# Optimization experiments

Measured on AMD Instinct MI355X. Metric: run time of the kernel, lower is better.

Reference implementation:

```python
import jax, jax.numpy as jnp
import numpy as np

N = 4096   # nodes
G = 64     # graphs
MH = 128   # hidden multiplicity (0e and 1o)
MU = 64    # up multiplicity (0e and 1o)
NSP = 10   # num_species
EPS = 1e-5


def _forward(nfh, nfu, onehot, W_h0, W_h1, W_u0, W_u1, Wt_00, Wt_11, Wt_01, Wt_10,
             W_p0, b_p0, W_p1, Wsc0, Wsc1, ln_w0, ln_b0, ln_w1, W_s0, b_s0, W_s1, batch):
    n = nfh.shape[0]
    # unpack irreps layout: [0e scalars | 1o vectors flattened]
    h0 = nfh[:, :MH]                       # [N, MH]
    h1 = nfh[:, MH:].reshape(n, MH, 3)     # [N, MH, 3]
    u0 = nfu[:, :MU]
    u1 = nfu[:, MU:].reshape(n, MU, 3)
    inv_h = 1.0 / np.sqrt(MH)
    inv_u = 1.0 / np.sqrt(MU)
    # irrep-wise (block-diagonal) o3.Linear, e3nn fan-in normalization
    hp0 = (h0 @ W_h0) * inv_h
    hp1 = jnp.einsum('nui,uv->nvi', h1, W_h1) * inv_h
    up0 = (u0 @ W_u0) * inv_u
    up1 = jnp.einsum('nui,uv->nvi', u1, W_u1) * inv_u
    # SeparateWeightTensorProduct: fully-connected 'uvw' CG tensor product
    # paths to 0e (scalars + gates, 2*MH outputs): 0e x 0e and 1o x 1o (dot / sqrt3)
    inv_tp = 1.0 / np.sqrt(2.0 * MH * MU)   # component/path normalization (2 paths, fan MH*MU)
    xy00 = jnp.einsum('nu,nv->nuv', hp0, up0).reshape(n, MH * MU)
    xy11 = jnp.einsum('nui,nvi->nuv', hp1, up1).reshape(n, MH * MU)
    z0 = (xy00 @ Wt_00.reshape(MH * MU, 2 * MH)
          + (xy11 @ Wt_11.reshape(MH * MU, 2 * MH)) / np.sqrt(3.0)) * inv_tp  # [N, 2*MH]
    # paths to 1o: 0e x 1o and 1o x 0e (staged to control intermediate size)
    ta = jnp.einsum('nu,uvw->nvw', hp0, Wt_01)       # [N, MU, MH]
    z1a = jnp.einsum('nvw,nvi->nwi', ta, up1)
    tb = jnp.einsum('nv,uvw->nuw', up0, Wt_10)       # [N, MH, MH]
    z1b = jnp.einsum('nuw,nui->nwi', tb, hp1)
    z1 = (z1a + z1b) * inv_tp                        # [N, MH, 3]
    # Gate nonlinearity: silu on scalars, sigmoid gates multiply 1o features
    s = jax.nn.silu(z0[:, :MH])
    g = jax.nn.sigmoid(z0[:, MH:])
    v = z1 * g[:, :, None]
    # lin_post (biases on scalars only)
    p0 = (s @ W_p0) * inv_h + b_p0
    p1 = jnp.einsum('nui,uv->nvi', v, W_p1) * inv_h
    # self-connection: FullyConnectedTensorProduct(hidden, NSPx0e, out)
    inv_sc = 1.0 / np.sqrt(MH * NSP)
    sxy0 = jnp.einsum('nu,nv->nuv', h0, onehot).reshape(n, MH * NSP)
    y0 = p0 + (sxy0 @ Wsc0.reshape(MH * NSP, MH)) * inv_sc
    sxy1 = jnp.einsum('nui,nv->nuvi', h1, onehot).reshape(n, MH * NSP, 3)
    y1 = p1 + jnp.einsum('nki,kw->nwi', sxy1, Wsc1.reshape(MH * NSP, MH)) * inv_sc
    # e3LayerNorm: per-graph stats; mean-subtract scalars only, RMS-normalize per irrep
    ones = jnp.ones((n,), y0.dtype)
    cnt = jnp.maximum(jax.ops.segment_sum(ones, batch, num_segments=G), 1.0)[:, None]
    mean0 = (jax.ops.segment_sum(y0, batch, num_segments=G) / cnt).mean(axis=1)  # [G]
    f0 = y0 - mean0[batch][:, None]
    var0 = (jax.ops.segment_sum(f0 * f0, batch, num_segments=G) / cnt).mean(axis=1)
    f0 = f0 / (jnp.sqrt(var0)[batch][:, None] + EPS) * ln_w0 + ln_b0
    var1 = (jax.ops.segment_sum((y1 * y1).reshape(n, -1), batch, num_segments=G) / cnt).mean(axis=1)
    f1 = y1 / (jnp.sqrt(var1)[batch][:, None, None] + EPS) * ln_w1[None, :, None]
    # residual skip connection (o3.Linear with scalar bias)
    out0 = f0 + (h0 @ W_s0) * inv_h + b_s0
    out1 = f1 + jnp.einsum('nui,uv->nvi', h1, W_s1) * inv_h
    return jnp.concatenate([out0, out1.reshape(n, 3 * MH)], axis=1)  # [N, 512]


def setup_inputs() -> dict:
    key = jax.random.key(0)
    ks = jax.random.split(key, 20)
    f = lambda i, shape: jax.random.normal(ks[i], shape, dtype=jnp.float32)
    species = jax.random.randint(ks[0], (N,), 0, NSP)
    return {
        'node_feats_hidden': f(1, (N, 4 * MH)),
        'node_feats_up': f(2, (N, 4 * MU)),
        'node_one_hot': jax.nn.one_hot(species, NSP, dtype=jnp.float32),
        'batch': jnp.sort(jax.random.randint(ks[3], (N,), 0, G)),
        'W_h0': f(4, (MH, MH)), 'W_h1': f(5, (MH, MH)),
        'W_u0': f(6, (MU, MU)), 'W_u1': f(7, (MU, MU)),
        'Wt_00': f(8, (MH, MU, 2 * MH)), 'Wt_11': f(9, (MH, MU, 2 * MH)),
        'Wt_01': f(10, (MH, MU, MH)), 'Wt_10': f(11, (MH, MU, MH)),
        'W_p0': f(12, (MH, MH)), 'b_p0': jnp.zeros((MH,), jnp.float32), 'W_p1': f(13, (MH, MH)),
        'Wsc0': f(14, (MH, NSP, MH)), 'Wsc1': f(15, (MH, NSP, MH)),
        'ln_w0': jnp.ones((MH,), jnp.float32), 'ln_b0': jnp.zeros((MH,), jnp.float32),
        'ln_w1': jnp.ones((MH,), jnp.float32),
        'W_s0': f(16, (MH, MH)), 'b_s0': jnp.zeros((MH,), jnp.float32), 'W_s1': f(17, (MH, MH)),
    }


def reference(node_feats_hidden, node_feats_up, node_one_hot, batch, W_h0, W_h1, W_u0, W_u1,
              Wt_00, Wt_11, Wt_01, Wt_10, W_p0, b_p0, W_p1, Wsc0, Wsc1, ln_w0, ln_b0, ln_w1,
              W_s0, b_s0, W_s1):
    return _forward(node_feats_hidden, node_feats_up, node_one_hot, W_h0, W_h1, W_u0, W_u1,
                    Wt_00, Wt_11, Wt_01, Wt_10, W_p0, b_p0, W_p1, Wsc0, Wsc1,
                    ln_w0, ln_b0, ln_w1, W_s0, b_s0, W_s1, batch)
```

## Files before the change

### kernel.cpp

```cpp
#include <hip/hip_runtime.h>
#include <cstdint>
#include <cstddef>


typedef _Float16 half8 __attribute__((ext_vector_type(8)));
typedef _Float16 half4v __attribute__((ext_vector_type(4)));
typedef float f32x4 __attribute__((ext_vector_type(4)));

static constexpr float INV_H  = 0.08838834764831845f;
static constexpr float INV_U  = 0.125f;
static constexpr float INV_TP = 0.0078125f;
static constexpr float INV_SC = 0.02795084971874737f;
static constexpr float RSQRT3 = 0.5773502691896258f;
static constexpr float LN_EPS = 1e-5f;

static constexpr size_t OFF_BZ0 = 0;
static constexpr size_t OFF_BZ1 = OFF_BZ0 + 8388608;
static constexpr size_t OFF_WH0 = OFF_BZ1 + 4194304;
static constexpr size_t OFF_WH1 = OFF_WH0 + 32768;
static constexpr size_t OFF_WU0 = OFF_WH1 + 32768;
static constexpr size_t OFF_WU1 = OFF_WU0 + 8192;
static constexpr size_t OFF_WP0 = OFF_WU1 + 8192;
static constexpr size_t OFF_WP1 = OFF_WP0 + 32768;
static constexpr size_t OFF_WS0 = OFF_WP1 + 32768;
static constexpr size_t OFF_WS1 = OFF_WS0 + 32768;
static constexpr size_t OFF_H0F = OFF_WS1 + 32768;
static constexpr size_t OFF_H1F = OFF_H0F + 1048576;
static constexpr size_t OFF_U0F = OFF_H1F + 3145728;
static constexpr size_t OFF_U1F = OFF_U0F + 524288;
static constexpr size_t OFF_HP0 = OFF_U1F + 1572864;
static constexpr size_t OFF_HP1 = OFF_HP0 + 1048576;
static constexpr size_t OFF_UP0 = OFF_HP1 + 3145728;
static constexpr size_t OFF_UP1 = OFF_UP0 + 524288;
static constexpr size_t OFF_SF  = OFF_UP1 + 1572864;
static constexpr size_t OFF_VF  = OFF_SF + 1048576;
static constexpr size_t OFF_PZ0 = OFF_VF + 3145728;
static constexpr size_t OFF_PZ1 = OFF_PZ0 + 16777216;
static constexpr size_t OFF_Y0  = OFF_PZ1 + 12582912;
static constexpr size_t OFF_Y1  = OFF_Y0 + 2097152;
static constexpr size_t OFF_O0  = OFF_Y1 + 6291456;
static constexpr size_t OFF_O1  = OFF_O0 + 2097152;
static constexpr size_t OFF_SP  = OFF_O1 + 6291456;
static constexpr size_t OFF_ST  = OFF_SP + 16384;
static constexpr size_t WS_NEED = OFF_ST + 2048;

__global__ __launch_bounds__(256) void kconv(
    const float* __restrict__ nfh, const float* __restrict__ nfu,
    const float* __restrict__ onehot,
    const float* __restrict__ Wt00, const float* __restrict__ Wt11,
    const float* __restrict__ Wt01, const float* __restrict__ Wt10,
    const float* __restrict__ Wh0, const float* __restrict__ Wh1,
    const float* __restrict__ Wu0, const float* __restrict__ Wu1,
    const float* __restrict__ Wp0, const float* __restrict__ Wp1,
    const float* __restrict__ Ws0, const float* __restrict__ Ws1,
    char* __restrict__ ws)
{
  const int bid = blockIdx.x, t = threadIdx.x;
  if (bid < 768) {
    __shared__ float lds[64 * 130];
    _Float16* dst;
    int u, nt = 0;
    const bool isz0 = bid < 512;
    if (isz0) { nt = bid >> 8; u = bid & 255; dst = (_Float16*)(ws + OFF_BZ0) + ((size_t)nt*256 + (size_t)u)*8192; }
    else      { u = bid - 512;               dst = (_Float16*)(ws + OFF_BZ1) + (size_t)u*8192; }

    const float* src; int rowpitch, c0; float scale = 1.f;
    if (isz0) {
      rowpitch = 256; c0 = nt*128;
      if (u < 128) { src = Wt00 + (size_t)(u*64)*256; }
      else         { src = Wt11 + (size_t)((u-128)*64)*256; scale = RSQRT3; }
    } else {
      rowpitch = 128; c0 = 0;
      if (u < 128) { src = Wt01 + (size_t)(u*64)*128; }
      else         { src = Wt10 + (size_t)((u-128)*64)*128; }
    }

    #pragma unroll
    for (int it = 0; it < 8; ++it) {
      int gi = it*256 + t;
      int row = gi >> 5, c4 = gi & 31;
      const float4 v = *(const float4*)(src + (size_t)row*rowpitch + c0 + c4*4);
      float* dl = lds + row*130 + c4*4;
      dl[0] = v.x; dl[1] = v.y; dl[2] = v.z; dl[3] = v.w;
    }
    __syncthreads();

    for (int it = 0; it < 4; ++it) {
      int chunk = it*256 + t;
      int lane = chunk & 63, ch = chunk >> 6;
      int f = ch >> 1, c = ch & 1;
      int w = f*16 + (lane & 15);
      int v0 = c*32 + (lane >> 4)*8;
      half8 o;
      #pragma unroll
      for (int j = 0; j < 8; ++j)
        o[j] = (_Float16)(lds[(v0 + j)*130 + w] * scale);
      *(half8*)(dst + (size_t)chunk*8) = o;
    }
  } else if (bid < 776) {
    int mat = bid - 768;
    const float* src; size_t doff; int K, N;
    switch (mat) {
      case 0: src = Wh0; doff = OFF_WH0; K = 128; N = 128; break;
      case 1: src = Wh1; doff = OFF_WH1; K = 128; N = 128; break;
      case 2: src = Wu0; doff = OFF_WU0; K = 64;  N = 64;  break;
      case 3: src = Wu1; doff = OFF_WU1; K = 64;  N = 64;  break;
      case 4: src = Wp0; doff = OFF_WP0; K = 128; N = 128; break;
      case 5: src = Wp1; doff = OFF_WP1; K = 128; N = 128; break;
      case 6: src = Ws0; doff = OFF_WS0; K = 128; N = 128; break;
      default: src = Ws1; doff = OFF_WS1; K = 128; N = 128; break;
    }
    _Float16* d = (_Float16*)(ws + doff);
    const int nfr = N >> 4;
    const int chunks = (K*N) >> 3;
    for (int qd = t; qd < chunks; qd += 256) {
      int lane = qd & 63, cf = qd >> 6;
      int f = cf % nfr, c = cf / nfr;
      int col = f*16 + (lane & 15);
      int k0 = c*32 + (lane >> 4)*8;
      half8 o;
      #pragma unroll
      for (int j = 0; j < 8; ++j) o[j] = (_Float16)src[(size_t)(k0 + j)*N + col];
      *(half8*)(d + (size_t)qd*8) = o;
    }
  } else if (bid < 1544) {
    const int stride = 768*256;
    const int base = (bid - 776)*256 + t;
    _Float16* h0f = (_Float16*)(ws + OFF_H0F);
    _Float16* h1f = (_Float16*)(ws + OFF_H1F);
    _Float16* u0f = (_Float16*)(ws + OFF_U0F);
    _Float16* u1f = (_Float16*)(ws + OFF_U1F);
    for (int vid = base; vid < 131072; vid += stride) {
      int n = vid >> 5, c4 = (vid & 31)*4;
      const float4 v = *(const float4*)(nfh + (size_t)n*512 + c4);
      half4v o = { (_Float16)v.x, (_Float16)v.y, (_Float16)v.z, (_Float16)v.w };
      *(half4v*)(h0f + (size_t)vid*4) = o;
    }
    for (int vid = base; vid < 65536; vid += stride) {
      int n = vid >> 4, c4 = (vid & 15)*4;
      const float4 v = *(const float4*)(nfu + (size_t)n*256 + c4);
      half4v o = { (_Float16)v.x, (_Float16)v.y, (_Float16)v.z, (_Float16)v.w };
      *(half4v*)(u0f + (size_t)vid*4) = o;
    }
    for (int id = base; id < 524288; id += stride) {
      int n = id >> 7, u = id & 127;
      const float* s = nfh + (size_t)n*512 + 128 + u*3;
      h1f[id]            = (_Float16)s[0];
      h1f[524288 + id]   = (_Float16)s[1];
      h1f[1048576 + id]  = (_Float16)s[2];
    }
    for (int id = base; id < 262144; id += stride) {
      int n = id >> 6, v = id & 63;
      const float* s = nfu + (size_t)n*256 + 64 + v*3;
      u1f[id]            = (_Float16)s[0];
      u1f[262144 + id]   = (_Float16)s[1];
      u1f[524288 + id]   = (_Float16)s[2];
    }
  } else {
    int node = (bid - 1544)*256 + t;
    const float* row = onehot + (size_t)node*10;
    int best = 0; float bv = row[0];
    #pragma unroll
    for (int s = 1; s < 10; ++s) { float v = row[s]; if (v > bv) { bv = v; best = s; } }
    ((int*)(ws + OFF_SP))[node] = best;
    if (bid == 1544) {
      float* stz = (float*)(ws + OFF_ST);
      stz[t] = 0.f; stz[t + 256] = 0.f;
    }
  }
}

template<int KK, int NO, int MODE>
__device__ __forceinline__ void gemm_small_body(char* __restrict__ ws,
    const float* __restrict__ bp0, const float* __restrict__ bs0,
    int bid, int t)
{
  constexpr int NT = NO / 16;
  const int lane = t & 63, wid = t >> 6;
  const int quad = lane >> 4, l15 = lane & 15;
  const int job = bid >> 5, n0 = (bid & 31) << 7;

  const _Float16 *A, *W;
  _Float16* oh = nullptr; float* of = nullptr;
  const float* bias = nullptr;
  float scale;
  if constexpr (MODE == 0) {
    scale = INV_H;
    if (job == 0) { A = (const _Float16*)(ws + OFF_H0F); W = (const _Float16*)(ws + OFF_WH0); oh = (_Float16*)(ws + OFF_HP0); }
    else {
      A = (const _Float16*)(ws + OFF_H1F) + (size_t)(job-1)*524288;
      W = (const _Float16*)(ws + OFF_WH1);
      oh = (_Float16*)(ws + OFF_HP1) + (size_t)(job-1)*524288;
    }
  } else if constexpr (MODE == 1) {
    scale = INV_U;
    if (job == 0) { A = (const _Float16*)(ws + OFF_U0F); W = (const _Float16*)(ws + OFF_WU0); oh = (_Float16*)(ws + OFF_UP0); }
    else {
      A = (const _Float16*)(ws + OFF_U1F) + (size_t)(job-1)*262144;
      W = (const _Float16*)(ws + OFF_WU1);
      oh = (_Float16*)(ws + OFF_UP1) + (size_t)(job-1)*262144;
    }
  } else {
    scale = INV_H;
    switch (job) {
      case 0: A = (const _Float16*)(ws + OFF_SF);  W = (const _Float16*)(ws + OFF_WP0); of = (float*)(ws + OFF_Y0); bias = bp0; break;
      case 1: A = (const _Float16*)(ws + OFF_H0F); W = (const _Float16*)(ws + OFF_WS0); of = (float*)(ws + OFF_O0); bias = bs0; break;
      case 2: case 3: case 4:
        A = (const _Float16*)(ws + OFF_VF) + (size_t)(job-2)*524288;
        W = (const _Float16*)(ws + OFF_WP1);
        of = (float*)(ws + OFF_Y1) + (size_t)(job-2)*524288; break;
      default:
        A = (const _Float16*)(ws + OFF_H1F) + (size_t)(job-5)*524288;
        W = (const _Float16*)(ws + OFF_WS1);
        of = (float*)(ws + OFF_O1) + (size_t)(job-5)*524288; break;
    }
  }

  f32x4 acc[2][NT];
  const f32x4 zz = {0.f, 0.f, 0.f, 0.f};
  #pragma unroll
  for (int mf = 0; mf < 2; ++mf)
    #pragma unroll
    for (int nf = 0; nf < NT; ++nf) acc[mf][nf] = zz;

  #pragma unroll
  for (int kc = 0; kc < KK/32; ++kc) {
    half8 a[2];
    #pragma unroll
    for (int mf = 0; mf < 2; ++mf)
      a[mf] = *(const half8*)(A + (size_t)(n0 + wid*32 + mf*16 + l15)*KK + kc*32 + quad*8);
    #pragma unroll
    for (int nf = 0; nf < NT; ++nf) {
      half8 b = *(const half8*)(W + (size_t)(kc*NT + nf)*512 + lane*8);
      #pragma unroll
      for (int mf = 0; mf < 2; ++mf)
        acc[mf][nf] = __builtin_amdgcn_mfma_f32_16x16x32_f16(a[mf], b, acc[mf][nf], 0, 0, 0);
    }
  }

  #pragma unroll
  for (int mf = 0; mf < 2; ++mf)
    #pragma unroll
    for (int nf = 0; nf < NT; ++nf) {
      int col = nf*16 + l15;
      float bv = bias ? bias[col] : 0.f;
      #pragma unroll
      for (int r = 0; r < 4; ++r) {
        int row = n0 + wid*32 + mf*16 + quad*4 + r;
        float v = acc[mf][nf][r] * scale + bv;
        if constexpr (MODE < 2) oh[(size_t)row*NO + col] = (_Float16)v;
        else                    of[(size_t)row*NO + col] = v;
      }
    }
}

__global__ __launch_bounds__(256) void kprep(char* __restrict__ ws)
{
  if (blockIdx.x < 128) gemm_small_body<128,128,0>(ws, nullptr, nullptr, blockIdx.x, threadIdx.x);
  else                  gemm_small_body<64, 64, 1>(ws, nullptr, nullptr, blockIdx.x - 128, threadIdx.x);
}

__global__ __launch_bounds__(256) void ktail(char* __restrict__ ws,
    const float* __restrict__ bp0, const float* __restrict__ bs0)
{
  gemm_small_body<128,128,2>(ws, bp0, bs0, blockIdx.x, threadIdx.x);
}

__global__ __launch_bounds__(256, 2) void kbig(char* __restrict__ ws)
{
  const int bid = blockIdx.x, t = threadIdx.x;
  const int lane = t & 63, wid = t >> 6;
  const int wy = wid >> 1, wx = wid & 1;
  const int quad = lane >> 4, l15 = lane & 15;

  const _Float16* hp0 = (const _Float16*)(ws + OFF_HP0);
  const _Float16* hp1 = (const _Float16*)(ws + OFF_HP1);
  const _Float16* up0 = (const _Float16*)(ws + OFF_UP0);
  const _Float16* up1 = (const _Float16*)(ws + OFF_UP1);

  const _Float16 *p, *q, *B0;
  _Float16* out; int opitch; size_t obase; int node0;
  if (bid < 256) {
    int mt = bid >> 3, nt = (bid >> 2) & 1, kj = bid & 3;
    node0 = mt << 7;
    if (kj == 0) { p = hp0; q = up0; }
    else { p = hp1 + (size_t)(kj-1)*524288; q = up1 + (size_t)(kj-1)*262144; }
    B0 = (const _Float16*)(ws + OFF_BZ0) + (size_t)nt*2097152 + (kj ? (size_t)1048576 : (size_t)0);
    out = (_Float16*)(ws + OFF_PZ0) + (size_t)kj*1048576;
    obase = (size_t)node0*256 + (size_t)nt*128;
    opitch = 256;
  } else {
    int b2 = bid - 256, mt = b2 >> 1, kj = b2 & 1, i = mt >> 5;
    node0 = (mt & 31) << 7;
    if (kj == 0) { p = hp0; q = up1 + (size_t)i*262144; }
    else         { p = hp1 + (size_t)i*524288; q = up0; }
    B0 = (const _Float16*)(ws + OFF_BZ1) + (kj ? (size_t)1048576 : (size_t)0);
    out = (_Float16*)(ws + OFF_PZ1) + (size_t)kj*1572864;
    obase = (size_t)mt*16384;
    opitch = 128;
  }

  half8 qf[4][2];
  #pragma unroll
  for (int mf = 0; mf < 4; ++mf)
    #pragma unroll
    for (int c = 0; c < 2; ++c)
      qf[mf][c] = *(const half8*)(q + (size_t)(node0 + wy*64 + mf*16 + l15)*64 + c*32 + quad*8);

  f32x4 acc[4][4];
  const f32x4 zz = {0.f, 0.f, 0.f, 0.f};
  #pragma unroll
  for (int mf = 0; mf < 4; ++mf)
    #pragma unroll
    for (int nf = 0; nf < 4; ++nf) acc[mf][nf] = zz;

  const _Float16* prow = p + (size_t)(node0 + wy*64 + l15)*128;
  const _Float16* Bw = B0 + (size_t)wx*4096 + (size_t)lane*8;

  for (int u4 = 0; u4 < 32; ++u4) {
    half4v pw[4];
    #pragma unroll
    for (int mf = 0; mf < 4; ++mf)
      pw[mf] = *(const half4v*)(prow + (size_t)mf*2048 + u4*4);
    #pragma unroll
    for (int uu = 0; uu < 4; ++uu) {
      const _Float16* Bu = Bw + (size_t)(u4*4 + uu)*8192;
      half8 bf[2][4];
      #pragma unroll
      for (int c = 0; c < 2; ++c)
        #pragma unroll
        for (int nf = 0; nf < 4; ++nf)
          bf[c][nf] = *(const half8*)(Bu + (size_t)((nf*2 + c)*512));
      #pragma unroll
      for (int mf = 0; mf < 4; ++mf) {
        const _Float16 ps = pw[mf][uu];
        const half8 pv = {ps, ps, ps, ps, ps, ps, ps, ps};
        #pragma unroll
        for (int c = 0; c < 2; ++c) {
          half8 a = qf[mf][c] * pv;
          #pragma unroll
          for (int nf = 0; nf < 4; ++nf)
            acc[mf][nf] = __builtin_amdgcn_mfma_f32_16x16x32_f16(a, bf[c][nf], acc[mf][nf], 0, 0, 0);
        }
      }
    }
  }

  #pragma unroll
  for (int mf = 0; mf < 4; ++mf)
    #pragma unroll
    for (int nf = 0; nf < 4; ++nf) {
      int col = wx*64 + nf*16 + l15;
      #pragma unroll
      for (int r = 0; r < 4; ++r) {
        int row = wy*64 + mf*16 + quad*4 + r;
        out[obase + (size_t)row*opitch + col] = (_Float16)acc[mf][nf][r];
      }
    }
}

__global__ __launch_bounds__(256) void kreduce(char* __restrict__ ws)
{
  const int id = blockIdx.x*256 + threadIdx.x;
  const int n = id >> 7, w = id & 127;
  const _Float16* pz0 = (const _Float16*)(ws + OFF_PZ0);
  const _Float16* pz1 = (const _Float16*)(ws + OFF_PZ1);
  _Float16* sf = (_Float16*)(ws + OFF_SF);
  _Float16* vf = (_Float16*)(ws + OFF_VF);
  const size_t b = (size_t)n*256;
  float zs = ((float)pz0[b + w] + (float)pz0[1048576 + b + w]
            + (float)pz0[2097152 + b + w] + (float)pz0[3145728 + b + w]) * INV_TP;
  float zg = ((float)pz0[b + 128 + w] + (float)pz0[1048576 + b + 128 + w]
            + (float)pz0[2097152 + b + 128 + w] + (float)pz0[3145728 + b + 128 + w]) * INV_TP;
  float s = zs / (1.f + __expf(-zs));
  float g = 1.f / (1.f + __expf(-zg));
  sf[id] = (_Float16)s;
  #pragma unroll
  for (int i = 0; i < 3; ++i) {
    size_t r = ((size_t)i*4096 + (size_t)n)*128 + w;
    float z1v = ((float)pz1[r] + (float)pz1[1572864 + r]) * INV_TP;
    vf[(size_t)i*524288 + (size_t)n*128 + w] = (_Float16)(z1v * g);
  }
}

__global__ __launch_bounds__(256) void kscstats(char* __restrict__ ws,
    const float* __restrict__ nfh,
    const float* __restrict__ Wsc0, const float* __restrict__ Wsc1,
    const int* __restrict__ batch)
{
  const int t = threadIdx.x;
  const int node = blockIdx.x*2 + (t >> 7);
  const int w = t & 127;
  const int sp = ((const int*)(ws + OFF_SP))[node];
  const float* h = nfh + (size_t)node*512;
  float a0 = 0.f, a10 = 0.f, a11 = 0.f, a12 = 0.f;
  for (int u = 0; u < 128; ++u) {
    const size_t wi = (size_t)(u*10 + sp)*128 + w;
    float w0 = Wsc0[wi];
    float w1 = Wsc1[wi];
    a0 += h[u] * w0;
    a10 += h[128 + u*3 + 0] * w1;
    a11 += h[128 + u*3 + 1] * w1;
    a12 += h[128 + u*3 + 2] * w1;
  }
  float* y0 = (float*)(ws + OFF_Y0);
  float* y1 = (float*)(ws + OFF_Y1);
  const size_t i0 = (size_t)node*128 + w;
  float y0n  = y0[i0]           + INV_SC * a0;
  float y1n0 = y1[i0]           + INV_SC * a10;
  float y1n1 = y1[524288 + i0]  + INV_SC * a11;
  float y1n2 = y1[1048576 + i0] + INV_SC * a12;
  y0[i0] = y0n;
  y1[i0] = y1n0;
  y1[524288 + i0]  = y1n1;
  y1[1048576 + i0] = y1n2;

  float s0 = y0n, ss0 = y0n*y0n, ss1 = y1n0*y1n0 + y1n1*y1n1 + y1n2*y1n2;
  #pragma unroll
  for (int m = 1; m < 64; m <<= 1) {
    s0  += __shfl_xor(s0, m, 64);
    ss0 += __shfl_xor(ss0, m, 64);
    ss1 += __shfl_xor(ss1, m, 64);
  }
  __shared__ float red[4][3];
  if ((t & 63) == 0) {
    red[t >> 6][0] = s0; red[t >> 6][1] = ss0; red[t >> 6][2] = ss1;
  }
  __syncthreads();
  if ((t & 127) == 0) {
    const int wv = t >> 6;
    float* stp = (float*)(ws + OFF_ST);
    const int g = batch[node];
    atomicAdd(&stp[g],       red[wv][0] + red[wv+1][0]);
    atomicAdd(&stp[64 + g],  red[wv][1] + red[wv+1][1]);
    atomicAdd(&stp[128 + g], red[wv][2] + red[wv+1][2]);
    atomicAdd(&stp[192 + g], 1.f);
  }
}

__global__ __launch_bounds__(256) void kfinal(char* __restrict__ ws, const int* __restrict__ batch,
    const float* __restrict__ lnw0, const float* __restrict__ lnb0, const float* __restrict__ lnw1,
    float* __restrict__ outp)
{
  const int id = blockIdx.x*256 + threadIdx.x;
  const int n = id >> 9, c = id & 511;
  const float* st = (const float*)(ws + OFF_ST);
  const int g = batch[n];
  const float cnt = fmaxf(st[192 + g], 1.f);
  float val;
  if (c < 128) {
    const float* y0 = (const float*)(ws + OFF_Y0);
    const float* o0 = (const float*)(ws + OFF_O0);
    float m0   = st[g] / (cnt * 128.f);
    float var0 = st[64 + g] / (cnt * 128.f) - m0*m0;
    float inv0 = 1.f / (sqrtf(fmaxf(var0, 0.f)) + LN_EPS);
    val = (y0[(size_t)n*128 + c] - m0) * inv0 * lnw0[c] + lnb0[c] + o0[(size_t)n*128 + c];
  } else {
    int cc = c - 128, w = cc / 3, i = cc - w*3;
    const float* y1 = (const float*)(ws + OFF_Y1);
    const float* o1 = (const float*)(ws + OFF_O1);
    float inv1 = 1.f / (sqrtf(fmaxf(st[128 + g] / (cnt * 384.f), 0.f)) + LN_EPS);
    val = y1[(size_t)i*524288 + (size_t)n*128 + w] * inv1 * lnw1[w]
        + o1[(size_t)i*524288 + (size_t)n*128 + w];
  }
  outp[id] = val;
}

extern "C" void kernel_launch(void* const* d_in, const int* in_sizes, int n_in,
                              void* d_out, int out_size, void* d_ws, size_t ws_size,
                              hipStream_t stream)
{
  const float* nfh   = (const float*)d_in[0];
  const float* nfu   = (const float*)d_in[1];
  const float* oneh  = (const float*)d_in[2];
  const int*   batch = (const int*)d_in[3];
  const float* Wh0   = (const float*)d_in[4];
  const float* Wh1   = (const float*)d_in[5];
  const float* Wu0   = (const float*)d_in[6];
  const float* Wu1   = (const float*)d_in[7];
  const float* Wt00  = (const float*)d_in[8];
  const float* Wt11  = (const float*)d_in[9];
  const float* Wt01  = (const float*)d_in[10];
  const float* Wt10  = (const float*)d_in[11];
  const float* Wp0   = (const float*)d_in[12];
  const float* bp0   = (const float*)d_in[13];
  const float* Wp1   = (const float*)d_in[14];
  const float* Wsc0  = (const float*)d_in[15];
  const float* Wsc1  = (const float*)d_in[16];
  const float* lnw0  = (const float*)d_in[17];
  const float* lnb0  = (const float*)d_in[18];
  const float* lnw1  = (const float*)d_in[19];
  const float* Ws0   = (const float*)d_in[20];
  const float* bs0   = (const float*)d_in[21];
  const float* Ws1   = (const float*)d_in[22];
  char* ws = (char*)d_ws;

  if (ws_size < WS_NEED) {
    hipMemsetAsync(d_out, 0, (size_t)out_size * sizeof(float), stream);
    return;
  }

  kconv<<<1560, 256, 0, stream>>>(nfh, nfu, oneh, Wt00, Wt11, Wt01, Wt10,
                                  Wh0, Wh1, Wu0, Wu1, Wp0, Wp1, Ws0, Ws1, ws);
  kprep<<<256, 256, 0, stream>>>(ws);
  kbig<<<448, 256, 0, stream>>>(ws);
  kreduce<<<2048, 256, 0, stream>>>(ws);
  ktail<<<256, 256, 0, stream>>>(ws, bp0, bs0);
  kscstats<<<2048, 256, 0, stream>>>(ws, nfh, Wsc0, Wsc1, batch);
  kfinal<<<8192, 256, 0, stream>>>(ws, batch, lnw0, lnb0, lnw1, (float*)d_out);
}
```

Measured before the change: 341.6 us.

## Software-pipeline B-fragment loads with inline asm double buffering and manual vmcnt waits

Rewrites the inner loop of the factored tensor-product MFMA kernel so that B-weight fragments and p scalars are loaded with inline global_load asm into two alternating register buffers, prefetching one u-step ahead. Explicit s_waitcnt vmcnt counts and sched_barrier control when data must arrive, so global load latency overlaps with MFMA work. This costs more VGPRs for the double buffers, and the hand-counted vmcnt values are fragile: a wrong count would read stale data.

```diff
diff --git a/kernel.cpp b/kernel.cpp
--- a/kernel.cpp
+++ b/kernel.cpp
@@ -315,36 +315,64 @@
     for (int nf = 0; nf < 4; ++nf) acc[mf][nf] = zz;
 
   const _Float16* prow = p + (size_t)(node0 + wy*64 + l15)*128;
-  const _Float16* Bw = B0 + (size_t)wx*4096 + (size_t)lane*8;
-
-  for (int u4 = 0; u4 < 32; ++u4) {
-    half4v pw[4];
+  const char* Bw = (const char*)(B0 + (size_t)wx*4096 + (size_t)lane*8);
+
+  half8 bufA[8], bufB[8];
+  half4v pwA[4], pwB[4];
+
+  auto LDB = [&](half8 (&buf)[8], int uidx) {
+    const char* b  = Bw + (size_t)uidx*16384;
+    const char* b2 = b + 4096;
+    asm volatile("global_load_dwordx4 %0, %1, off"             : "=v"(buf[0]) : "v"(b));
+    asm volatile("global_load_dwordx4 %0, %1, off offset:1024" : "=v"(buf[1]) : "v"(b));
+    asm volatile("global_load_dwordx4 %0, %1, off offset:2048" : "=v"(buf[2]) : "v"(b));
+    asm volatile("global_load_dwordx4 %0, %1, off offset:3072" : "=v"(buf[3]) : "v"(b));
+    asm volatile("global_load_dwordx4 %0, %1, off"             : "=v"(buf[4]) : "v"(b2));
+    asm volatile("global_load_dwordx4 %0, %1, off offset:1024" : "=v"(buf[5]) : "v"(b2));
+    asm volatile("global_load_dwordx4 %0, %1, off offset:2048" : "=v"(buf[6]) : "v"(b2));
+    asm volatile("global_load_dwordx4 %0, %1, off offset:3072" : "=v"(buf[7]) : "v"(b2));
+  };
+  auto LDP = [&](half4v (&pp)[4], int u4n) {
     #pragma unroll
     for (int mf = 0; mf < 4; ++mf)
-      pw[mf] = *(const half4v*)(prow + (size_t)mf*2048 + u4*4);
-    #pragma unroll
-    for (int uu = 0; uu < 4; ++uu) {
-      const _Float16* Bu = Bw + (size_t)(u4*4 + uu)*8192;
-      half8 bf[2][4];
+      asm volatile("global_load_dwordx2 %0, %1, off"
+                   : "=v"(pp[mf]) : "v"(prow + (size_t)mf*2048 + u4n*4));
+  };
+  auto MSTEP = [&](half8 (&buf)[8], half4v (&pp)[4], int uu, int deep) {
+    if (deep) asm volatile("s_waitcnt vmcnt(12)" ::: "memory");
+    else      asm volatile("s_waitcnt vmcnt(8)"  ::: "memory");
+    __builtin_amdgcn_sched_barrier(0);
+    half8 av[4][2];
+    #pragma unroll
+    for (int mf = 0; mf < 4; ++mf) {
+      const _Float16 ps = pp[mf][uu];
+      const half8 pv = {ps, ps, ps, ps, ps, ps, ps, ps};
+      #pragma unroll
+      for (int c = 0; c < 2; ++c) av[mf][c] = qf[mf][c] * pv;
+    }
+    #pragma unroll
+    for (int mf = 0; mf < 4; ++mf)
       #pragma unroll
       for (int c = 0; c < 2; ++c)
         #pragma unroll
         for (int nf = 0; nf < 4; ++nf)
-          bf[c][nf] = *(const half8*)(Bu + (size_t)((nf*2 + c)*512));
-      #pragma unroll
-      for (int mf = 0; mf < 4; ++mf) {
-        const _Float16 ps = pw[mf][uu];
-        const half8 pv = {ps, ps, ps, ps, ps, ps, ps, ps};
-        #pragma unroll
-        for (int c = 0; c < 2; ++c) {
-          half8 a = qf[mf][c] * pv;
-          #pragma unroll
-          for (int nf = 0; nf < 4; ++nf)
-            acc[mf][nf] = __builtin_amdgcn_mfma_f32_16x16x32_f16(a, bf[c][nf], acc[mf][nf], 0, 0, 0);
-        }
-      }
-    }
-  }
+          acc[mf][nf] = __builtin_amdgcn_mfma_f32_16x16x32_f16(av[mf][c], buf[nf*2 + c], acc[mf][nf], 0, 0, 0);
+  };
+
+  LDB(bufA, 0);
+  LDP(pwA, 0);
+  for (int pn = 0; pn < 16; ++pn) {
+    const int b = pn*8;
+    LDB(bufB, b+1);                                  MSTEP(bufA, pwA, 0, 0);
+    LDB(bufA, b+2);                                  MSTEP(bufB, pwA, 1, 0);
+    LDB(bufB, b+3); LDP(pwB, pn*2+1);                MSTEP(bufA, pwA, 2, 1);
+    LDB(bufA, b+4);                                  MSTEP(bufB, pwA, 3, 1);
+    LDB(bufB, b+5);                                  MSTEP(bufA, pwB, 0, 0);
+    LDB(bufA, b+6);                                  MSTEP(bufB, pwB, 1, 0);
+    LDB(bufB, b+7); LDP(pwA, (pn < 15) ? pn*2+2 : 31); MSTEP(bufA, pwB, 2, 1);
+    LDB(bufA, (pn < 15) ? b+8 : 127);                MSTEP(bufB, pwB, 3, 1);
+  }
+  asm volatile("s_waitcnt vmcnt(0)" ::: "memory");
 
   #pragma unroll
   for (int mf = 0; mf < 4; ++mf)
```

New measurement: 336.2 us. Within noise of the previous version (-1.6%).

## Retile kbig to 256-node tiles with hand-pipelined triple-buffered B loads

Applied to the files above, without the earlier changes.

Each kbig block now covers 256 nodes by 64 output columns instead of 128 by 128. Each wave handles 128 rows and 32 columns, so more A rows are reused per B fragment. The main loop is replaced by a fully unrolled software pipeline: inline-asm global loads triple-buffer the B fragments and double-buffer the p scalars, with explicit vmcnt waits and sched barriers so loads overlap the MFMAs. The aim is to hide global load latency and cut B traffic per FLOP, at the cost of more registers and fragile hand-counted waitcnts.

```diff
diff --git a/kernel.cpp b/kernel.cpp
--- a/kernel.cpp
+++ b/kernel.cpp
@@ -281,79 +281,127 @@
   const _Float16 *p, *q, *B0;
   _Float16* out; int opitch; size_t obase; int node0;
   if (bid < 256) {
-    int mt = bid >> 3, nt = (bid >> 2) & 1, kj = bid & 3;
-    node0 = mt << 7;
+    const int mt2 = bid >> 4, cs = (bid >> 2) & 3, kj = bid & 3;
+    node0 = mt2 << 8;
     if (kj == 0) { p = hp0; q = up0; }
     else { p = hp1 + (size_t)(kj-1)*524288; q = up1 + (size_t)(kj-1)*262144; }
-    B0 = (const _Float16*)(ws + OFF_BZ0) + (size_t)nt*2097152 + (kj ? (size_t)1048576 : (size_t)0);
+    const int nt = cs >> 1, csl = cs & 1;
+    B0 = (const _Float16*)(ws + OFF_BZ0) + (size_t)nt*2097152 + (kj ? (size_t)1048576 : (size_t)0)
+       + (size_t)csl*4096;
     out = (_Float16*)(ws + OFF_PZ0) + (size_t)kj*1048576;
-    obase = (size_t)node0*256 + (size_t)nt*128;
+    obase = (size_t)node0*256 + (size_t)cs*64;
     opitch = 256;
   } else {
-    int b2 = bid - 256, mt = b2 >> 1, kj = b2 & 1, i = mt >> 5;
-    node0 = (mt & 31) << 7;
+    const int b2 = bid - 256, mt2 = b2 >> 2, cs = (b2 >> 1) & 1, kj = b2 & 1;
+    const int i = mt2 >> 4;
+    node0 = (mt2 & 15) << 8;
     if (kj == 0) { p = hp0; q = up1 + (size_t)i*262144; }
     else         { p = hp1 + (size_t)i*524288; q = up0; }
-    B0 = (const _Float16*)(ws + OFF_BZ1) + (kj ? (size_t)1048576 : (size_t)0);
+    B0 = (const _Float16*)(ws + OFF_BZ1) + (kj ? (size_t)1048576 : (size_t)0) + (size_t)cs*4096;
     out = (_Float16*)(ws + OFF_PZ1) + (size_t)kj*1572864;
-    obase = (size_t)mt*16384;
+    obase = ((size_t)i*4096 + (size_t)node0)*128 + (size_t)cs*64;
     opitch = 128;
   }
 
-  half8 qf[4][2];
-  #pragma unroll
-  for (int mf = 0; mf < 4; ++mf)
+  half8 qf[8][2];
+  #pragma unroll
+  for (int mf = 0; mf < 8; ++mf)
     #pragma unroll
     for (int c = 0; c < 2; ++c)
-      qf[mf][c] = *(const half8*)(q + (size_t)(node0 + wy*64 + mf*16 + l15)*64 + c*32 + quad*8);
-
-  f32x4 acc[4][4];
+      qf[mf][c] = *(const half8*)(q + (size_t)(node0 + wy*128 + mf*16 + l15)*64 + c*32 + quad*8);
+
+  f32x4 acc[8][2];
   const f32x4 zz = {0.f, 0.f, 0.f, 0.f};
   #pragma unroll
-  for (int mf = 0; mf < 4; ++mf)
-    #pragma unroll
-    for (int nf = 0; nf < 4; ++nf) acc[mf][nf] = zz;
-
-  const _Float16* prow = p + (size_t)(node0 + wy*64 + l15)*128;
-  const _Float16* Bw = B0 + (size_t)wx*4096 + (size_t)lane*8;
-
-  for (int u4 = 0; u4 < 32; ++u4) {
-    half4v pw[4];
-    #pragma unroll
-    for (int mf = 0; mf < 4; ++mf)
-      pw[mf] = *(const half4v*)(prow + (size_t)mf*2048 + u4*4);
-    #pragma unroll
-    for (int uu = 0; uu < 4; ++uu) {
-      const _Float16* Bu = Bw + (size_t)(u4*4 + uu)*8192;
-      half8 bf[2][4];
-      #pragma unroll
-      for (int c = 0; c < 2; ++c)
-        #pragma unroll
-        for (int nf = 0; nf < 4; ++nf)
-          bf[c][nf] = *(const half8*)(Bu + (size_t)((nf*2 + c)*512));
-      #pragma unroll
-      for (int mf = 0; mf < 4; ++mf) {
-        const _Float16 ps = pw[mf][uu];
-        const half8 pv = {ps, ps, ps, ps, ps, ps, ps, ps};
-        #pragma unroll
-        for (int c = 0; c < 2; ++c) {
-          half8 a = qf[mf][c] * pv;
-          #pragma unroll
-          for (int nf = 0; nf < 4; ++nf)
-            acc[mf][nf] = __builtin_amdgcn_mfma_f32_16x16x32_f16(a, bf[c][nf], acc[mf][nf], 0, 0, 0);
-        }
-      }
-    }
-  }
-
-  #pragma unroll
-  for (int mf = 0; mf < 4; ++mf)
-    #pragma unroll
-    for (int nf = 0; nf < 4; ++nf) {
-      int col = wx*64 + nf*16 + l15;
+  for (int mf = 0; mf < 8; ++mf)
+    #pragma unroll
+    for (int nf = 0; nf < 2; ++nf) acc[mf][nf] = zz;
+
+  const _Float16* prow = p + (size_t)(node0 + wy*128 + l15)*128;
+  const char* Bw = (const char*)(B0 + (size_t)wx*2048 + (size_t)lane*8);
+
+  half8 b0[4], b1[4], b2[4];
+  half4v pwA[8], pwB[8];
+
+  auto LDB = [&](half8 (&buf)[4], int uidx) {
+    const char* b = Bw + (size_t)uidx*16384;
+    asm volatile("global_load_dwordx4 %0, %1, off"             : "=v"(buf[0]) : "v"(b));
+    asm volatile("global_load_dwordx4 %0, %1, off offset:1024" : "=v"(buf[1]) : "v"(b));
+    asm volatile("global_load_dwordx4 %0, %1, off offset:2048" : "=v"(buf[2]) : "v"(b));
+    asm volatile("global_load_dwordx4 %0, %1, off offset:3072" : "=v"(buf[3]) : "v"(b));
+  };
+  auto LDP = [&](half4v (&pp)[8], int u4n) {
+    #pragma unroll
+    for (int mf = 0; mf < 8; ++mf)
+      asm volatile("global_load_dwordx2 %0, %1, off"
+                   : "=v"(pp[mf]) : "v"(prow + (size_t)mf*2048 + u4n*4));
+  };
+  auto MSTEP = [&](half8 (&buf)[4], half4v (&pp)[8], int uu, int nwait) {
+    if      (nwait == 16) asm volatile("s_waitcnt vmcnt(16)" ::: "memory");
+    else if (nwait == 8)  asm volatile("s_waitcnt vmcnt(8)"  ::: "memory");
+    else if (nwait == 4)  asm volatile("s_waitcnt vmcnt(4)"  ::: "memory");
+    else                  asm volatile("s_waitcnt vmcnt(0)"  ::: "memory");
+    __builtin_amdgcn_sched_barrier(0);
+    #pragma unroll
+    for (int mf = 0; mf < 8; ++mf) {
+      const _Float16 ps = pp[mf][uu];
+      const half8 pv = {ps, ps, ps, ps, ps, ps, ps, ps};
+      half8 av0 = qf[mf][0] * pv;
+      half8 av1 = qf[mf][1] * pv;
+      acc[mf][0] = __builtin_amdgcn_mfma_f32_16x16x32_f16(av0, buf[0], acc[mf][0], 0, 0, 0);
+      acc[mf][1] = __builtin_amdgcn_mfma_f32_16x16x32_f16(av0, buf[2], acc[mf][1], 0, 0, 0);
+      acc[mf][0] = __builtin_amdgcn_mfma_f32_16x16x32_f16(av1, buf[1], acc[mf][0], 0, 0, 0);
+      acc[mf][1] = __builtin_amdgcn_mfma_f32_16x16x32_f16(av1, buf[3], acc[mf][1], 0, 0, 0);
+    }
+  };
+
+  LDP(pwA, 0);
+  LDB(b0, 0); LDB(b1, 1); LDB(b2, 2);
+
+  for (int pn = 0; pn < 5; ++pn) {
+    const int s0 = pn*24, w0 = pn*6;
+    MSTEP(b0, pwA, 0, 8);  LDB(b0, s0+3);  LDP(pwB, w0+1);
+    MSTEP(b1, pwA, 1, 16); LDB(b1, s0+4);
+    MSTEP(b2, pwA, 2, 16); LDB(b2, s0+5);
+    MSTEP(b0, pwA, 3, 16); LDB(b0, s0+6);
+    MSTEP(b1, pwB, 0, 8);  LDB(b1, s0+7);  LDP(pwA, w0+2);
+    MSTEP(b2, pwB, 1, 16); LDB(b2, s0+8);
+    MSTEP(b0, pwB, 2, 16); LDB(b0, s0+9);
+    MSTEP(b1, pwB, 3, 16); LDB(b1, s0+10);
+    MSTEP(b2, pwA, 0, 8);  LDB(b2, s0+11); LDP(pwB, w0+3);
+    MSTEP(b0, pwA, 1, 16); LDB(b0, s0+12);
+    MSTEP(b1, pwA, 2, 16); LDB(b1, s0+13);
+    MSTEP(b2, pwA, 3, 16); LDB(b2, s0+14);
+    MSTEP(b0, pwB, 0, 8);  LDB(b0, s0+15); LDP(pwA, w0+4);
+    MSTEP(b1, pwB, 1, 16); LDB(b1, s0+16);
+    MSTEP(b2, pwB, 2, 16); LDB(b2, s0+17);
+    MSTEP(b0, pwB, 3, 16); LDB(b0, s0+18);
+    MSTEP(b1, pwA, 0, 8);  LDB(b1, s0+19); LDP(pwB, w0+5);
+    MSTEP(b2, pwA, 1, 16); LDB(b2, s0+20);
+    MSTEP(b0, pwA, 2, 16); LDB(b0, s0+21);
+    MSTEP(b1, pwA, 3, 16); LDB(b1, s0+22);
+    MSTEP(b2, pwB, 0, 8);  LDB(b2, s0+23); LDP(pwA, (pn < 4) ? w0+6 : 30);
+    MSTEP(b0, pwB, 1, 16); LDB(b0, s0+24);
+    MSTEP(b1, pwB, 2, 16); LDB(b1, s0+25);
+    MSTEP(b2, pwB, 3, 16); LDB(b2, s0+26);
+  }
+  MSTEP(b0, pwA, 0, 8);  LDB(b0, 123); LDP(pwB, 31);
+  MSTEP(b1, pwA, 1, 16); LDB(b1, 124);
+  MSTEP(b2, pwA, 2, 16); LDB(b2, 125);
+  MSTEP(b0, pwA, 3, 16); LDB(b0, 126);
+  MSTEP(b1, pwB, 0, 8);  LDB(b1, 127);
+  MSTEP(b2, pwB, 1, 8);
+  MSTEP(b0, pwB, 2, 4);
+  MSTEP(b1, pwB, 3, 0);
+
+  #pragma unroll
+  for (int mf = 0; mf < 8; ++mf)
+    #pragma unroll
+    for (int nf = 0; nf < 2; ++nf) {
+      int col = wx*32 + nf*16 + l15;
       #pragma unroll
       for (int r = 0; r < 4; ++r) {
-        int row = wy*64 + mf*16 + quad*4 + r;
+        int row = wy*128 + mf*16 + quad*4 + r;
         out[obase + (size_t)row*opitch + col] = (_Float16)acc[mf][nf][r];
       }
     }
```

After: 343.3 us. Within noise of the previous version (+0.5%).

## Double-buffer B weight slices in LDS via async global_load_lds

Applied to the files above, without the earlier changes.

Each u-step's B weight slice, previously read by every wave directly from global memory, is now staged cooperatively into a double-buffered LDS tile using global_load_lds. The next slice loads while the current one feeds the MFMAs. This removes redundant global/L2 traffic across waves sharing the same B slice. The cost is a __syncthreads per u-step, 32KB of LDS per block (which may lower occupancy), and reliance on the async LDS load completing before the barrier.

```diff
diff --git a/kernel.cpp b/kernel.cpp
--- a/kernel.cpp
+++ b/kernel.cpp
@@ -315,34 +315,60 @@
     for (int nf = 0; nf < 4; ++nf) acc[mf][nf] = zz;
 
   const _Float16* prow = p + (size_t)(node0 + wy*64 + l15)*128;
-  const _Float16* Bw = B0 + (size_t)wx*4096 + (size_t)lane*8;
-
+  const char* Bt = (const char*)B0;
+
+  __shared__ _Float16 Bs[2][8192];
+  _Float16* lb0 = &Bs[0][0];
+  _Float16* lb1 = &Bs[1][0];
+
+  auto STAGE = [&](_Float16* lb, int u) {
+    const char* src = Bt + (size_t)u*16384;
+    #pragma unroll
+    for (int i = 0; i < 4; ++i) {
+      const int off = (wid*4 + i)*1024;
+      __builtin_amdgcn_global_load_lds(
+          (const uint32_t*)(src + off + lane*16),
+          (uint32_t*)((char*)lb + off), 16, 0, 0);
+    }
+  };
+  auto MSTEP = [&](const _Float16* lb, const half4v (&pp)[4], int uu) {
+    const _Float16* Bl = lb + wx*4096 + lane*8;
+    half8 bf[2][4];
+    #pragma unroll
+    for (int c = 0; c < 2; ++c)
+      #pragma unroll
+      for (int nf = 0; nf < 4; ++nf)
+        bf[c][nf] = *(const half8*)(Bl + (size_t)((nf*2 + c)*512));
+    #pragma unroll
+    for (int mf = 0; mf < 4; ++mf) {
+      const _Float16 ps = pp[mf][uu];
+      const half8 pv = {ps, ps, ps, ps, ps, ps, ps, ps};
+      #pragma unroll
+      for (int c = 0; c < 2; ++c) {
+        half8 a = qf[mf][c] * pv;
+        #pragma unroll
+        for (int nf = 0; nf < 4; ++nf)
+          acc[mf][nf] = __builtin_amdgcn_mfma_f32_16x16x32_f16(a, bf[c][nf], acc[mf][nf], 0, 0, 0);
+      }
+    }
+  };
+
+  STAGE(lb0, 0);
+  __syncthreads();
+
+  half4v pw[4];
   for (int u4 = 0; u4 < 32; ++u4) {
-    half4v pw[4];
     #pragma unroll
     for (int mf = 0; mf < 4; ++mf)
       pw[mf] = *(const half4v*)(prow + (size_t)mf*2048 + u4*4);
     #pragma unroll
     for (int uu = 0; uu < 4; ++uu) {
-      const _Float16* Bu = Bw + (size_t)(u4*4 + uu)*8192;
-      half8 bf[2][4];
-      #pragma unroll
-      for (int c = 0; c < 2; ++c)
-        #pragma unroll
-        for (int nf = 0; nf < 4; ++nf)
-          bf[c][nf] = *(const half8*)(Bu + (size_t)((nf*2 + c)*512));
-      #pragma unroll
-      for (int mf = 0; mf < 4; ++mf) {
-        const _Float16 ps = pw[mf][uu];
-        const half8 pv = {ps, ps, ps, ps, ps, ps, ps, ps};
-        #pragma unroll
-        for (int c = 0; c < 2; ++c) {
-          half8 a = qf[mf][c] * pv;
-          #pragma unroll
-          for (int nf = 0; nf < 4; ++nf)
-            acc[mf][nf] = __builtin_amdgcn_mfma_f32_16x16x32_f16(a, bf[c][nf], acc[mf][nf], 0, 0, 0);
-        }
-      }
+      const int u = u4*4 + uu;
+      _Float16* lcur = (uu & 1) ? lb1 : lb0;
+      _Float16* lnxt = (uu & 1) ? lb0 : lb1;
+      if (u < 127) STAGE(lnxt, u + 1);
+      MSTEP(lcur, pw, uu);
+      __syncthreads();
     }
   }
 
```

New measurement: 342.7 us. Within noise of the previous version (+0.3%).
